# Optimization experiments

Measured on AMD Instinct MI355X. Metric: run time of the kernel, lower is better.

Reference implementation:

```python
import jax, jax.numpy as jnp
import numpy as np

D_MODEL = 512
D_INNER = 1024   # 2 * d_model (Mamba default expand=2)
D_STATE = 16
D_CONV = 4
DT_RANK = 32     # ceil(d_model / 16)
N_LAYERS = 2
EPS = 1e-5


def rmsnorm(x, w):
    return x * jax.lax.rsqrt(jnp.mean(x * x, axis=-1, keepdims=True) + EPS) * w


def silu(x):
    return x * jax.nn.sigmoid(x)


def causal_conv1d(x, w, b):
    # x: [B,S,di], w: [di,d_conv] depthwise, b: [di]; causal left padding
    xt = jnp.transpose(x, (0, 2, 1))                 # [B,di,S]
    k = w[:, None, :]                                # [di,1,k]
    y = jax.lax.conv_general_dilated(
        xt, k, (1,), [(D_CONV - 1, 0)],
        dimension_numbers=('NCH', 'OIH', 'NCH'),
        feature_group_count=D_INNER)
    return jnp.transpose(y, (0, 2, 1)) + b


def selective_scan(u, dt, A, Bm, C, Dp):
    # u,dt: [B,S,di]; Bm,C: [B,S,ds]; A: [di,ds]; Dp: [di]
    def step(h, inp):
        dt_t, B_t, C_t, u_t = inp                    # [B,di],[B,ds],[B,ds],[B,di]
        dA = jnp.exp(dt_t[:, :, None] * A)           # [B,di,ds]
        h = dA * h + (dt_t * u_t)[:, :, None] * B_t[:, None, :]
        y = jnp.einsum('bds,bs->bd', h, C_t)
        return h, y

    B, S, di = u.shape
    h0 = jnp.zeros((B, di, D_STATE), u.dtype)
    xs = (jnp.swapaxes(dt, 0, 1), jnp.swapaxes(Bm, 0, 1),
          jnp.swapaxes(C, 0, 1), jnp.swapaxes(u, 0, 1))
    _, ys = jax.lax.scan(step, h0, xs)               # ys: [S,B,di]
    return jnp.swapaxes(ys, 0, 1) + u * Dp


def mamba_block(x, in_proj, conv_w, conv_b, xproj, dtproj, dtproj_b, A_log, Dp, outproj):
    xz = x @ in_proj.T                               # [B,S,2*di]
    u, z = jnp.split(xz, 2, axis=-1)
    u = silu(causal_conv1d(u, conv_w, conv_b))
    x_dbl = u @ xproj.T                              # [B,S,dt_rank+2*ds]
    dt = jax.nn.softplus(x_dbl[..., :DT_RANK] @ dtproj.T + dtproj_b)
    Bm = x_dbl[..., DT_RANK:DT_RANK + D_STATE]
    C = x_dbl[..., DT_RANK + D_STATE:]
    A = -jnp.exp(A_log)
    y = selective_scan(u, dt, A, Bm, C, Dp)
    return (y * silu(z)) @ outproj.T


def setup_inputs() -> dict:
    key = jax.random.key(0)
    ks = jax.random.split(key, 8)
    B, S, L = 2, 2048, N_LAYERS

    def w(k, shape, s=0.02):
        return jax.random.normal(k, shape, jnp.float32) * s

    inp = {}
    inp['input_data'] = jax.random.normal(ks[0], (B, D_MODEL, S), jnp.float32)
    inp['mask'] = jnp.ones((B, S), jnp.bool_)
    inp['in_proj_w'] = w(ks[1], (L, 2 * D_INNER, D_MODEL))
    inp['conv_w'] = w(ks[2], (L, D_INNER, D_CONV), 0.2)
    inp['conv_b'] = jnp.zeros((L, D_INNER), jnp.float32)
    inp['xproj_w'] = w(ks[3], (L, DT_RANK + 2 * D_STATE, D_INNER))
    inp['dtproj_w'] = w(ks[4], (L, D_INNER, DT_RANK), 0.1)
    inp['dtproj_b'] = w(ks[5], (L, D_INNER), 0.5) - 4.0  # softplus -> small dt
    inp['A_log'] = jnp.log(jnp.broadcast_to(
        jnp.arange(1, D_STATE + 1, dtype=jnp.float32), (L, D_INNER, D_STATE)))
    inp['Dp'] = jnp.ones((L, D_INNER), jnp.float32)
    inp['outproj_w'] = w(ks[6], (L, D_MODEL, D_INNER))
    inp['norm_w'] = jnp.ones((L, D_MODEL), jnp.float32)
    inp['final_norm_w'] = jnp.ones((D_MODEL,), jnp.float32)
    return inp


def reference(input_data, mask, in_proj_w, conv_w, conv_b, xproj_w, dtproj_w,
              dtproj_b, A_log, Dp, outproj_w, norm_w, final_norm_w):
    x = jnp.transpose(input_data, (0, 2, 1))         # [B,S,D]
    for l in range(N_LAYERS):
        x = x + mamba_block(rmsnorm(x, norm_w[l]), in_proj_w[l], conv_w[l],
                            conv_b[l], xproj_w[l], dtproj_w[l], dtproj_b[l],
                            A_log[l], Dp[l], outproj_w[l])
    tokens = rmsnorm(x, final_norm_w)                # [B,S,D] (lm_head=Identity)
    lengths = jnp.sum(mask.astype(jnp.int32), axis=1)
    idx = jnp.maximum(lengths - 1, 0)
    emb = jnp.take_along_axis(tokens, idx[:, None, None], axis=1)[:, 0]  # [B,D]
    return tokens, emb
```

## Files before the change

### kernel.cpp

```cpp
#include <hip/hip_runtime.h>
#include <hip/hip_bf16.h>
#include <cmath>

#define BQ 2
#define SQ 2048
#define DM 512
#define DI 1024
#define DSTATE 16
#define DCONV 4
#define DTR 32
#define NLAYERS 2
#define CHUNK 64
#define NCH (SQ / CHUNK)

typedef __attribute__((ext_vector_type(8))) short bf16x8;
typedef __attribute__((ext_vector_type(4))) float f32x4;

__device__ __forceinline__ unsigned short f2bf(float f) {
    __hip_bfloat16 h = __float2bfloat16(f);
    return *reinterpret_cast<unsigned short*>(&h);
}

__global__ __launch_bounds__(256) void k_transpose(const float* __restrict__ in,
                                                   float* __restrict__ out) {
    __shared__ float tile[32][33];
    int b = blockIdx.z;
    int s0 = blockIdx.x * 32, c0 = blockIdx.y * 32;
    int tx = threadIdx.x, ty = threadIdx.y;
#pragma unroll
    for (int i = 0; i < 4; i++)
        tile[ty + i * 8][tx] = in[((size_t)b * DM + c0 + ty + i * 8) * SQ + s0 + tx];
    __syncthreads();
#pragma unroll
    for (int i = 0; i < 4; i++)
        out[((size_t)b * SQ + s0 + ty + i * 8) * DM + c0 + tx] = tile[tx][ty + i * 8];
}

__global__ __launch_bounds__(256) void k_cvt(const float* __restrict__ in,
                                             unsigned short* __restrict__ out, int n4) {
    int i = blockIdx.x * 256 + threadIdx.x;
    if (i >= n4) return;
    float4 v = ((const float4*)in)[i];
    ushort4 o;
    o.x = f2bf(v.x); o.y = f2bf(v.y); o.z = f2bf(v.z); o.w = f2bf(v.w);
    ((ushort4*)out)[i] = o;
}

__global__ __launch_bounds__(256) void k_rmsnorm_bf(const float* __restrict__ x,
                                                    const float* __restrict__ w,
                                                    unsigned short* __restrict__ out) {
    int row = blockIdx.x;
    const float* xr = x + (size_t)row * DM;
    float v0 = xr[threadIdx.x];
    float v1 = xr[threadIdx.x + 256];
    float ss = v0 * v0 + v1 * v1;
#pragma unroll
    for (int off = 32; off >= 1; off >>= 1) ss += __shfl_xor(ss, off);
    __shared__ float wc[4];
    if ((threadIdx.x & 63) == 0) wc[threadIdx.x >> 6] = ss;
    __syncthreads();
    ss = wc[0] + wc[1] + wc[2] + wc[3];
    float r = rsqrtf(ss * (1.0f / DM) + 1e-5f);
    out[(size_t)row * DM + threadIdx.x] = f2bf(v0 * r * w[threadIdx.x]);
    out[(size_t)row * DM + threadIdx.x + 256] = f2bf(v1 * r * w[threadIdx.x + 256]);
}

__global__ __launch_bounds__(256) void k_rmsnorm_f32(const float* __restrict__ x,
                                                     const float* __restrict__ w,
                                                     float* __restrict__ out) {
    int row = blockIdx.x;
    const float* xr = x + (size_t)row * DM;
    float v0 = xr[threadIdx.x];
    float v1 = xr[threadIdx.x + 256];
    float ss = v0 * v0 + v1 * v1;
#pragma unroll
    for (int off = 32; off >= 1; off >>= 1) ss += __shfl_xor(ss, off);
    __shared__ float wc[4];
    if ((threadIdx.x & 63) == 0) wc[threadIdx.x >> 6] = ss;
    __syncthreads();
    ss = wc[0] + wc[1] + wc[2] + wc[3];
    float r = rsqrtf(ss * (1.0f / DM) + 1e-5f);
    out[(size_t)row * DM + threadIdx.x] = v0 * r * w[threadIdx.x];
    out[(size_t)row * DM + threadIdx.x + 256] = v1 * r * w[threadIdx.x + 256];
}

__global__ __launch_bounds__(256) void k_gemm_bf16(const unsigned short* __restrict__ A, int lda,
                                                   const unsigned short* __restrict__ W, int ldw,
                                                   float* __restrict__ C, int ldc, int K,
                                                   const float* __restrict__ resid, int ldr) {
    __shared__ __align__(16) unsigned short As[128 * 32];
    __shared__ __align__(16) unsigned short Bs[128 * 32];
    const int bm = blockIdx.y * 128, bn = blockIdx.x * 128;
    const int tid = threadIdx.x;
    const int w = tid >> 6, l = tid & 63;
    const int wr = w >> 1, wc = w & 1;
    const int lg = l >> 4, lr16 = l & 15;
    f32x4 acc[4][4] = {};
    for (int k0 = 0; k0 < K; k0 += 32) {
        __syncthreads();
#pragma unroll
        for (int i = 0; i < 2; i++) {
            int slot = i * 256 + tid;
            int row = slot >> 2, s = slot & 3;
            int sg = s ^ (row & 3);
            __builtin_amdgcn_global_load_lds(
                (const __attribute__((address_space(1))) unsigned int*)(A + (size_t)(bm + row) * lda + k0 + sg * 8),
                (__attribute__((address_space(3))) unsigned int*)(As + slot * 8), 16, 0, 0);
            __builtin_amdgcn_global_load_lds(
                (const __attribute__((address_space(1))) unsigned int*)(W + (size_t)(bn + row) * ldw + k0 + sg * 8),
                (__attribute__((address_space(3))) unsigned int*)(Bs + slot * 8), 16, 0, 0);
        }
        asm volatile("s_waitcnt vmcnt(0)" ::: "memory");
        __syncthreads();
        bf16x8 fa[4], fb[4];
#pragma unroll
        for (int f = 0; f < 4; f++) {
            int ar = wr * 64 + f * 16 + lr16;
            fa[f] = *(const bf16x8*)&As[ar * 32 + (lg ^ (ar & 3)) * 8];
            int br = wc * 64 + f * 16 + lr16;
            fb[f] = *(const bf16x8*)&Bs[br * 32 + (lg ^ (br & 3)) * 8];
        }
#pragma unroll
        for (int fi = 0; fi < 4; fi++)
#pragma unroll
            for (int fj = 0; fj < 4; fj++)
                acc[fi][fj] = __builtin_amdgcn_mfma_f32_16x16x32_bf16(fa[fi], fb[fj], acc[fi][fj], 0, 0, 0);
    }
#pragma unroll
    for (int fi = 0; fi < 4; fi++)
#pragma unroll
        for (int fj = 0; fj < 4; fj++)
#pragma unroll
            for (int r = 0; r < 4; r++) {
                int m = bm + wr * 64 + fi * 16 + lg * 4 + r;
                int n = bn + wc * 64 + fj * 16 + lr16;
                float v = acc[fi][fj][r];
                if (resid) v += resid[(size_t)m * ldr + n];
                C[(size_t)m * ldc + n] = v;
            }
}

__global__ __launch_bounds__(256) void k_gemm_bf16_n64(const unsigned short* __restrict__ A, int lda,
                                                       const unsigned short* __restrict__ W, int ldw,
                                                       float* __restrict__ C, int ldc, int K) {
    __shared__ __align__(16) unsigned short As[128 * 32];
    __shared__ __align__(16) unsigned short Bs[64 * 32];
    const int bm = blockIdx.x * 128;
    const int tid = threadIdx.x;
    const int w = tid >> 6, l = tid & 63;
    const int lg = l >> 4, lr16 = l & 15;
    f32x4 acc[2][4] = {};
    for (int k0 = 0; k0 < K; k0 += 32) {
        __syncthreads();
#pragma unroll
        for (int i = 0; i < 2; i++) {
            int slot = i * 256 + tid;
            int row = slot >> 2, s = slot & 3;
            int sg = s ^ (row & 3);
            __builtin_amdgcn_global_load_lds(
                (const __attribute__((address_space(1))) unsigned int*)(A + (size_t)(bm + row) * lda + k0 + sg * 8),
                (__attribute__((address_space(3))) unsigned int*)(As + slot * 8), 16, 0, 0);
        }
        {
            int slot = tid;
            int row = slot >> 2, s = slot & 3;
            int sg = s ^ (row & 3);
            __builtin_amdgcn_global_load_lds(
                (const __attribute__((address_space(1))) unsigned int*)(W + (size_t)row * ldw + k0 + sg * 8),
                (__attribute__((address_space(3))) unsigned int*)(Bs + slot * 8), 16, 0, 0);
        }
        asm volatile("s_waitcnt vmcnt(0)" ::: "memory");
        __syncthreads();
        bf16x8 fa[2], fb[4];
#pragma unroll
        for (int f = 0; f < 2; f++) {
            int ar = w * 32 + f * 16 + lr16;
            fa[f] = *(const bf16x8*)&As[ar * 32 + (lg ^ (ar & 3)) * 8];
        }
#pragma unroll
        for (int f = 0; f < 4; f++) {
            int br = f * 16 + lr16;
            fb[f] = *(const bf16x8*)&Bs[br * 32 + (lg ^ (br & 3)) * 8];
        }
#pragma unroll
        for (int fi = 0; fi < 2; fi++)
#pragma unroll
            for (int fj = 0; fj < 4; fj++)
                acc[fi][fj] = __builtin_amdgcn_mfma_f32_16x16x32_bf16(fa[fi], fb[fj], acc[fi][fj], 0, 0, 0);
    }
#pragma unroll
    for (int fi = 0; fi < 2; fi++)
#pragma unroll
        for (int fj = 0; fj < 4; fj++)
#pragma unroll
            for (int r = 0; r < 4; r++) {
                int m = bm + w * 32 + fi * 16 + lg * 4 + r;
                int n = fj * 16 + lr16;
                C[(size_t)m * ldc + n] = acc[fi][fj][r];
            }
}

__global__ __launch_bounds__(256) void k_gemm(const float* __restrict__ A, int lda,
                                              const float* __restrict__ W, int ldw,
                                              float* __restrict__ C, int ldc, int K,
                                              const float* __restrict__ bias, int act,
                                              const float* __restrict__ resid, int ldr) {
    __shared__ float As[16][64];
    __shared__ float Bs[16][64];
    int bm = blockIdx.y * 64, bn = blockIdx.x * 64;
    int tid = threadIdx.x;
    int tx = tid & 15, ty = tid >> 4;
    int lr = tid >> 2, lk = (tid & 3) << 2;
    float acc[4][4] = {};
    for (int k0 = 0; k0 < K; k0 += 16) {
        float4 av = *(const float4*)&A[(size_t)(bm + lr) * lda + k0 + lk];
        float4 wv = *(const float4*)&W[(size_t)(bn + lr) * ldw + k0 + lk];
        __syncthreads();
        As[lk + 0][lr] = av.x; As[lk + 1][lr] = av.y;
        As[lk + 2][lr] = av.z; As[lk + 3][lr] = av.w;
        Bs[lk + 0][lr] = wv.x; Bs[lk + 1][lr] = wv.y;
        Bs[lk + 2][lr] = wv.z; Bs[lk + 3][lr] = wv.w;
        __syncthreads();
#pragma unroll
        for (int k = 0; k < 16; k++) {
            float a[4], bb[4];
#pragma unroll
            for (int i = 0; i < 4; i++) a[i] = As[k][ty * 4 + i];
#pragma unroll
            for (int j = 0; j < 4; j++) bb[j] = Bs[k][tx * 4 + j];
#pragma unroll
            for (int i = 0; i < 4; i++)
#pragma unroll
                for (int j = 0; j < 4; j++) acc[i][j] += a[i] * bb[j];
        }
    }
#pragma unroll
    for (int i = 0; i < 4; i++) {
        int m = bm + ty * 4 + i;
#pragma unroll
        for (int j = 0; j < 4; j++) {
            int n = bn + tx * 4 + j;
            float v = acc[i][j];
            if (bias) v += bias[n];
            if (act == 1) v = fmaxf(v, 0.f) + log1pf(expf(-fabsf(v)));
            if (resid) v += resid[(size_t)m * ldr + n];
            C[(size_t)m * ldc + n] = v;
        }
    }
}

__global__ __launch_bounds__(256) void k_conv_silu(const float* __restrict__ xz,
                                                   const float* __restrict__ cw,
                                                   const float* __restrict__ cb,
                                                   float* __restrict__ u,
                                                   unsigned short* __restrict__ ubf) {
    int bt = blockIdx.x;
    int t = bt & (SQ - 1);
#pragma unroll
    for (int dd = 0; dd < 4; dd++) {
        int d = dd * 256 + threadIdx.x;
        float acc = cb[d];
#pragma unroll
        for (int k = 0; k < DCONV; k++) {
            int tk = t + k - (DCONV - 1);
            if (tk >= 0)
                acc += xz[((size_t)(bt + k - (DCONV - 1))) * (2 * DI) + d] * cw[d * DCONV + k];
        }
        float sig = 1.f / (1.f + expf(-acc));
        float v = acc * sig;
        u[(size_t)bt * DI + d] = v;
        ubf[(size_t)bt * DI + d] = f2bf(v);
    }
}

__global__ __launch_bounds__(256) void k_scan_p1(const float* __restrict__ xdbl,
                                                 const float* __restrict__ dt,
                                                 const float* __restrict__ u,
                                                 const float* __restrict__ A_log,
                                                 float* __restrict__ hend,
                                                 float* __restrict__ dchunk) {
    int bc = blockIdx.x >> 4;
    int d0 = (blockIdx.x & 15) << 6;
    int b = bc >> 5;
    int c = bc & (NCH - 1);
    int tid = threadIdx.x;
    int q = tid & 3, dl = tid >> 2;
    int d = d0 + dl;
    float4 av = *(const float4*)&A_log[((size_t)d << 4) + 4 * q];
    float a0 = -expf(av.x), a1 = -expf(av.y), a2 = -expf(av.z), a3 = -expf(av.w);
    float h0 = 0.f, h1 = 0.f, h2 = 0.f, h3 = 0.f, sumdt = 0.f;
    __shared__ float sdt[32][65], su[32][65];
    __shared__ __align__(16) float sB[32][16];
    int tbase = c * CHUNK;
    for (int t0 = 0; t0 < CHUNK; t0 += 32) {
        __syncthreads();
#pragma unroll
        for (int i = 0; i < 8; i++) {
            int e = i * 256 + tid;
            int tt = e >> 6, j = e & 63;
            size_t rowm = (size_t)(b * SQ + tbase + t0 + tt);
            sdt[tt][j] = dt[rowm * DI + d0 + j];
            su[tt][j]  = u[rowm * DI + d0 + j];
        }
#pragma unroll
        for (int i = 0; i < 2; i++) {
            int e = i * 256 + tid;
            int tt = e >> 4, j = e & 15;
            size_t rowm = (size_t)(b * SQ + tbase + t0 + tt);
            sB[tt][j] = xdbl[rowm * 64 + DTR + j];
        }
        __syncthreads();
        for (int tt = 0; tt < 32; tt++) {
            float dtv = sdt[tt][dl], uv = su[tt][dl];
            float dtu = dtv * uv;
            sumdt += dtv;
            float4 Bv = *(const float4*)&sB[tt][4 * q];
            h0 = __expf(dtv * a0) * h0 + dtu * Bv.x;
            h1 = __expf(dtv * a1) * h1 + dtu * Bv.y;
            h2 = __expf(dtv * a2) * h2 + dtu * Bv.z;
            h3 = __expf(dtv * a3) * h3 + dtu * Bv.w;
        }
    }
    size_t o = ((size_t)bc << 14) + ((size_t)d << 4) + 4 * q;
    *(float4*)&hend[o] = make_float4(h0, h1, h2, h3);
    *(float4*)&dchunk[o] = make_float4(__expf(a0 * sumdt), __expf(a1 * sumdt),
                                       __expf(a2 * sumdt), __expf(a3 * sumdt));
}

__global__ __launch_bounds__(256) void k_scan_p2(const float* __restrict__ hend,
                                                 const float* __restrict__ dchunk,
                                                 float* __restrict__ hstart) {
    int tid = blockIdx.x * 256 + threadIdx.x;
    int b = tid >> 14;
    int ds = tid & 16383;
    float h = 0.f;
#pragma unroll
    for (int c = 0; c < NCH; c++) {
        size_t o = (((size_t)(b * NCH + c)) << 14) + ds;
        hstart[o] = h;
        h = dchunk[o] * h + hend[o];
    }
}

__global__ __launch_bounds__(256) void k_scan_p3(const float* __restrict__ xdbl,
                                                 const float* __restrict__ dt,
                                                 const float* __restrict__ u,
                                                 const float* __restrict__ xz,
                                                 const float* __restrict__ A_log,
                                                 const float* __restrict__ Dp,
                                                 const float* __restrict__ hstart,
                                                 unsigned short* __restrict__ yout) {
    int bc = blockIdx.x >> 4;
    int d0 = (blockIdx.x & 15) << 6;
    int b = bc >> 5;
    int c = bc & (NCH - 1);
    int tid = threadIdx.x;
    int q = tid & 3, dl = tid >> 2;
    int d = d0 + dl;
    float4 av = *(const float4*)&A_log[((size_t)d << 4) + 4 * q];
    float a0 = -expf(av.x), a1 = -expf(av.y), a2 = -expf(av.z), a3 = -expf(av.w);
    size_t o = ((size_t)bc << 14) + ((size_t)d << 4) + 4 * q;
    float4 hv = *(const float4*)&hstart[o];
    float h0 = hv.x, h1 = hv.y, h2 = hv.z, h3 = hv.w;
    float Dv = Dp[d];
    __shared__ float sdt[32][65], su[32][65], sz[32][65];
    __shared__ __align__(16) float sBC[32][32];
    int tbase = c * CHUNK;
    for (int t0 = 0; t0 < CHUNK; t0 += 32) {
        __syncthreads();
#pragma unroll
        for (int i = 0; i < 8; i++) {
            int e = i * 256 + tid;
            int tt = e >> 6, j = e & 63;
            size_t rowm = (size_t)(b * SQ + tbase + t0 + tt);
            sdt[tt][j] = dt[rowm * DI + d0 + j];
            su[tt][j]  = u[rowm * DI + d0 + j];
            sz[tt][j]  = xz[rowm * (2 * DI) + DI + d0 + j];
        }
#pragma unroll
        for (int i = 0; i < 4; i++) {
            int e = i * 256 + tid;
            int tt = e >> 5, j = e & 31;
            size_t rowm = (size_t)(b * SQ + tbase + t0 + tt);
            sBC[tt][j] = xdbl[rowm * 64 + DTR + j];
        }
        __syncthreads();
        for (int tt = 0; tt < 32; tt++) {
            float dtv = sdt[tt][dl], uv = su[tt][dl];
            float dtu = dtv * uv;
            float4 Bv = *(const float4*)&sBC[tt][4 * q];
            float4 Cv = *(const float4*)&sBC[tt][16 + 4 * q];
            h0 = __expf(dtv * a0) * h0 + dtu * Bv.x;
            h1 = __expf(dtv * a1) * h1 + dtu * Bv.y;
            h2 = __expf(dtv * a2) * h2 + dtu * Bv.z;
            h3 = __expf(dtv * a3) * h3 + dtu * Bv.w;
            float y = h0 * Cv.x + h1 * Cv.y + h2 * Cv.z + h3 * Cv.w;
            y += __shfl_xor(y, 1);
            y += __shfl_xor(y, 2);
            if (q == 0) {
                y += uv * Dv;
                float zv = sz[tt][dl];
                float g = zv / (1.f + __expf(-zv));
                yout[(size_t)(b * SQ + tbase + t0 + tt) * DI + d] = f2bf(y * g);
            }
        }
    }
}

__global__ __launch_bounds__(256) void k_emb(const float* __restrict__ tokens,
                                             const int* __restrict__ mask,
                                             float* __restrict__ emb) {
    int b = blockIdx.x;
    int cnt = 0;
    for (int i = threadIdx.x; i < SQ; i += 256) cnt += mask[b * SQ + i] ? 1 : 0;
#pragma unroll
    for (int off = 32; off >= 1; off >>= 1) cnt += __shfl_xor(cnt, off);
    __shared__ int wc[4];
    if ((threadIdx.x & 63) == 0) wc[threadIdx.x >> 6] = cnt;
    __syncthreads();
    int total = wc[0] + wc[1] + wc[2] + wc[3];
    int idx = total > 0 ? total - 1 : 0;
    for (int i = threadIdx.x; i < DM; i += 256)
        emb[b * DM + i] = tokens[((size_t)b * SQ + idx) * DM + i];
}

extern "C" void kernel_launch(void* const* d_in, const int* in_sizes, int n_in,
                              void* d_out, int out_size, void* d_ws, size_t ws_size,
                              hipStream_t stream) {
    const float* input_data   = (const float*)d_in[0];
    const int*   mask         = (const int*)d_in[1];
    const float* in_proj_w    = (const float*)d_in[2];
    const float* conv_w       = (const float*)d_in[3];
    const float* conv_b       = (const float*)d_in[4];
    const float* xproj_w      = (const float*)d_in[5];
    const float* dtproj_w     = (const float*)d_in[6];
    const float* dtproj_b     = (const float*)d_in[7];
    const float* A_log        = (const float*)d_in[8];
    const float* Dp           = (const float*)d_in[9];
    const float* outproj_w    = (const float*)d_in[10];
    const float* norm_w       = (const float*)d_in[11];
    const float* final_norm_w = (const float*)d_in[12];
    float* out = (float*)d_out;

    const size_t M = (size_t)BQ * SQ;
    const size_t CS = (size_t)BQ * NCH * DI * DSTATE;
    float* x              = (float*)d_ws;
    unsigned short* xn_bf = (unsigned short*)(x + M * DM);
    float* xz             = (float*)(xn_bf + M * DM);
    float* u              = xz + M * 2 * DI;
    float* xdbl           = u + M * DI;
    float* dtb            = xdbl + M * 64;
    unsigned short* ubf   = (unsigned short*)(dtb + M * DI);
    unsigned short* ybf   = ubf + M * DI;
    float* hend           = (float*)(ybf + M * DI);
    float* dchunk         = hend + CS;
    float* hstart         = dchunk + CS;
    unsigned short* wbf_in  = (unsigned short*)(hstart + CS);
    unsigned short* wbf_out = wbf_in + (size_t)NLAYERS * 2 * DI * DM;
    unsigned short* wbf_x   = wbf_out + (size_t)NLAYERS * DM * DI;

    {
        int n4 = NLAYERS * 2 * DI * DM / 4;
        k_cvt<<<(n4 + 255) / 256, 256, 0, stream>>>(in_proj_w, wbf_in, n4);
        n4 = NLAYERS * DM * DI / 4;
        k_cvt<<<(n4 + 255) / 256, 256, 0, stream>>>(outproj_w, wbf_out, n4);
        n4 = NLAYERS * 64 * DI / 4;
        k_cvt<<<(n4 + 255) / 256, 256, 0, stream>>>(xproj_w, wbf_x, n4);
    }

    k_transpose<<<dim3(SQ / 32, DM / 32, BQ), dim3(32, 8), 0, stream>>>(input_data, x);

    for (int l = 0; l < NLAYERS; l++) {
        k_rmsnorm_bf<<<M, 256, 0, stream>>>(x, norm_w + (size_t)l * DM, xn_bf);
        k_gemm_bf16<<<dim3(2 * DI / 128, M / 128), 256, 0, stream>>>(
            xn_bf, DM, wbf_in + (size_t)l * 2 * DI * DM, DM, xz, 2 * DI, DM,
            nullptr, 0);
        k_conv_silu<<<M, 256, 0, stream>>>(xz, conv_w + (size_t)l * DI * DCONV,
                                           conv_b + (size_t)l * DI, u, ubf);
        k_gemm_bf16_n64<<<M / 128, 256, 0, stream>>>(
            ubf, DI, wbf_x + (size_t)l * 64 * DI, DI, xdbl, 64, DI);
        k_gemm<<<dim3(DI / 64, M / 64), 256, 0, stream>>>(
            xdbl, 64, dtproj_w + (size_t)l * DI * DTR, DTR, dtb, DI, DTR,
            dtproj_b + (size_t)l * DI, 1, nullptr, 0);
        k_scan_p1<<<BQ * NCH * (DI / 64), 256, 0, stream>>>(
            xdbl, dtb, u, A_log + (size_t)l * DI * DSTATE, hend, dchunk);
        k_scan_p2<<<(BQ * DI * DSTATE) / 256, 256, 0, stream>>>(hend, dchunk, hstart);
        k_scan_p3<<<BQ * NCH * (DI / 64), 256, 0, stream>>>(
            xdbl, dtb, u, xz, A_log + (size_t)l * DI * DSTATE, Dp + (size_t)l * DI,
            hstart, ybf);
        k_gemm_bf16<<<dim3(DM / 128, M / 128), 256, 0, stream>>>(
            ybf, DI, wbf_out + (size_t)l * DM * DI, DI, x, DM, DI,
            x, DM);
    }

    k_rmsnorm_f32<<<M, 256, 0, stream>>>(x, final_norm_w, out);
    k_emb<<<BQ, 256, 0, stream>>>(out, mask, out + M * DM);
}
```

Measured before the change: 468.6 us.

## Template bf16 MFMA GEMM, split-K x_proj, sliding-window conv, vectorized scan loads

```diff
diff --git a/kernel.cpp b/kernel.cpp
--- a/kernel.cpp
+++ b/kernel.cpp
@@ -12,6 +12,7 @@
 #define NLAYERS 2
 #define CHUNK 64
 #define NCH (SQ / CHUNK)
+#define LOG2E 1.4426950408889634f
 
 typedef __attribute__((ext_vector_type(8))) short bf16x8;
 typedef __attribute__((ext_vector_type(4))) float f32x4;
@@ -84,19 +85,87 @@
     out[(size_t)row * DM + threadIdx.x + 256] = v1 * r * w[threadIdx.x + 256];
 }
 
-__global__ __launch_bounds__(256) void k_gemm_bf16(const unsigned short* __restrict__ A, int lda,
-                                                   const unsigned short* __restrict__ W, int ldw,
-                                                   float* __restrict__ C, int ldc, int K,
-                                                   const float* __restrict__ resid, int ldr) {
-    __shared__ __align__(16) unsigned short As[128 * 32];
-    __shared__ __align__(16) unsigned short Bs[128 * 32];
-    const int bm = blockIdx.y * 128, bn = blockIdx.x * 128;
+template<int BM, int BN, int AFR, int BFR>
+__global__ __launch_bounds__(256) void k_gemm_bf16_t(const unsigned short* __restrict__ A, int lda,
+                                                     const unsigned short* __restrict__ W, int ldw,
+                                                     float* __restrict__ C, int ldc, int K,
+                                                     const float* __restrict__ bias, int act,
+                                                     const float* __restrict__ resid, int ldr) {
+    __shared__ __align__(16) unsigned short As[BM * 32];
+    __shared__ __align__(16) unsigned short Bs[BN * 32];
+    const int bm = blockIdx.y * BM, bn = blockIdx.x * BN;
     const int tid = threadIdx.x;
     const int w = tid >> 6, l = tid & 63;
     const int wr = w >> 1, wc = w & 1;
     const int lg = l >> 4, lr16 = l & 15;
-    f32x4 acc[4][4] = {};
+    f32x4 acc[AFR][BFR] = {};
     for (int k0 = 0; k0 < K; k0 += 32) {
+        __syncthreads();
+#pragma unroll
+        for (int i = 0; i < BM / 64; i++) {
+            int slot = i * 256 + tid;
+            int row = slot >> 2, s = slot & 3;
+            int sg = s ^ (row & 3);
+            __builtin_amdgcn_global_load_lds(
+                (const __attribute__((address_space(1))) unsigned int*)(A + (size_t)(bm + row) * lda + k0 + sg * 8),
+                (__attribute__((address_space(3))) unsigned int*)(As + slot * 8), 16, 0, 0);
+        }
+#pragma unroll
+        for (int i = 0; i < BN / 64; i++) {
+            int slot = i * 256 + tid;
+            int row = slot >> 2, s = slot & 3;
+            int sg = s ^ (row & 3);
+            __builtin_amdgcn_global_load_lds(
+                (const __attribute__((address_space(1))) unsigned int*)(W + (size_t)(bn + row) * ldw + k0 + sg * 8),
+                (__attribute__((address_space(3))) unsigned int*)(Bs + slot * 8), 16, 0, 0);
+        }
+        asm volatile("s_waitcnt vmcnt(0)" ::: "memory");
+        __syncthreads();
+        bf16x8 fa[AFR], fb[BFR];
+#pragma unroll
+        for (int f = 0; f < AFR; f++) {
+            int ar = wr * (BM / 2) + f * 16 + lr16;
+            fa[f] = *(const bf16x8*)&As[ar * 32 + (lg ^ (ar & 3)) * 8];
+        }
+#pragma unroll
+        for (int f = 0; f < BFR; f++) {
+            int br = wc * (BN / 2) + f * 16 + lr16;
+            fb[f] = *(const bf16x8*)&Bs[br * 32 + (lg ^ (br & 3)) * 8];
+        }
+#pragma unroll
+        for (int fi = 0; fi < AFR; fi++)
+#pragma unroll
+            for (int fj = 0; fj < BFR; fj++)
+                acc[fi][fj] = __builtin_amdgcn_mfma_f32_16x16x32_bf16(fa[fi], fb[fj], acc[fi][fj], 0, 0, 0);
+    }
+#pragma unroll
+    for (int fi = 0; fi < AFR; fi++)
+#pragma unroll
+        for (int fj = 0; fj < BFR; fj++)
+#pragma unroll
+            for (int r = 0; r < 4; r++) {
+                int m = bm + wr * (BM / 2) + fi * 16 + lg * 4 + r;
+                int n = bn + wc * (BN / 2) + fj * 16 + lr16;
+                float v = acc[fi][fj][r];
+                if (bias) v += bias[n];
+                if (act == 1) v = fmaxf(v, 0.f) + log1pf(expf(-fabsf(v)));
+                if (resid) v += resid[(size_t)m * ldr + n];
+                C[(size_t)m * ldc + n] = v;
+            }
+}
+
+__global__ __launch_bounds__(256) void k_gemm_n64_sk(const unsigned short* __restrict__ A, int lda,
+                                                     const unsigned short* __restrict__ W, int ldw,
+                                                     float* __restrict__ part) {
+    __shared__ __align__(16) unsigned short As[128 * 32];
+    __shared__ __align__(16) unsigned short Bs[64 * 32];
+    const int bm = blockIdx.x * 128;
+    const int koff = blockIdx.y * 128;
+    const int tid = threadIdx.x;
+    const int w = tid >> 6, l = tid & 63;
+    const int lg = l >> 4, lr16 = l & 15;
+    f32x4 acc[2][4] = {};
+    for (int k0 = koff; k0 < koff + 128; k0 += 32) {
         __syncthreads();
 #pragma unroll
         for (int i = 0; i < 2; i++) {
@@ -106,60 +175,6 @@
             __builtin_amdgcn_global_load_lds(
                 (const __attribute__((address_space(1))) unsigned int*)(A + (size_t)(bm + row) * lda + k0 + sg * 8),
                 (__attribute__((address_space(3))) unsigned int*)(As + slot * 8), 16, 0, 0);
-            __builtin_amdgcn_global_load_lds(
-                (const __attribute__((address_space(1))) unsigned int*)(W + (size_t)(bn + row) * ldw + k0 + sg * 8),
-                (__attribute__((address_space(3))) unsigned int*)(Bs + slot * 8), 16, 0, 0);
-        }
-        asm volatile("s_waitcnt vmcnt(0)" ::: "memory");
-        __syncthreads();
-        bf16x8 fa[4], fb[4];
-#pragma unroll
-        for (int f = 0; f < 4; f++) {
-            int ar = wr * 64 + f * 16 + lr16;
-            fa[f] = *(const bf16x8*)&As[ar * 32 + (lg ^ (ar & 3)) * 8];
-            int br = wc * 64 + f * 16 + lr16;
-            fb[f] = *(const bf16x8*)&Bs[br * 32 + (lg ^ (br & 3)) * 8];
-        }
-#pragma unroll
-        for (int fi = 0; fi < 4; fi++)
-#pragma unroll
-            for (int fj = 0; fj < 4; fj++)
-                acc[fi][fj] = __builtin_amdgcn_mfma_f32_16x16x32_bf16(fa[fi], fb[fj], acc[fi][fj], 0, 0, 0);
-    }
-#pragma unroll
-    for (int fi = 0; fi < 4; fi++)
-#pragma unroll
-        for (int fj = 0; fj < 4; fj++)
-#pragma unroll
-            for (int r = 0; r < 4; r++) {
-                int m = bm + wr * 64 + fi * 16 + lg * 4 + r;
-                int n = bn + wc * 64 + fj * 16 + lr16;
-                float v = acc[fi][fj][r];
-                if (resid) v += resid[(size_t)m * ldr + n];
-                C[(size_t)m * ldc + n] = v;
-            }
-}
-
-__global__ __launch_bounds__(256) void k_gemm_bf16_n64(const unsigned short* __restrict__ A, int lda,
-                                                       const unsigned short* __restrict__ W, int ldw,
-                                                       float* __restrict__ C, int ldc, int K) {
-    __shared__ __align__(16) unsigned short As[128 * 32];
-    __shared__ __align__(16) unsigned short Bs[64 * 32];
-    const int bm = blockIdx.x * 128;
-    const int tid = threadIdx.x;
-    const int w = tid >> 6, l = tid & 63;
-    const int lg = l >> 4, lr16 = l & 15;
-    f32x4 acc[2][4] = {};
-    for (int k0 = 0; k0 < K; k0 += 32) {
-        __syncthreads();
-#pragma unroll
-        for (int i = 0; i < 2; i++) {
-            int slot = i * 256 + tid;
-            int row = slot >> 2, s = slot & 3;
-            int sg = s ^ (row & 3);
-            __builtin_amdgcn_global_load_lds(
-                (const __attribute__((address_space(1))) unsigned int*)(A + (size_t)(bm + row) * lda + k0 + sg * 8),
-                (__attribute__((address_space(3))) unsigned int*)(As + slot * 8), 16, 0, 0);
         }
         {
             int slot = tid;
@@ -188,6 +203,7 @@
             for (int fj = 0; fj < 4; fj++)
                 acc[fi][fj] = __builtin_amdgcn_mfma_f32_16x16x32_bf16(fa[fi], fb[fj], acc[fi][fj], 0, 0, 0);
     }
+    float* out = part + (size_t)blockIdx.y * ((size_t)BQ * SQ * 64);
 #pragma unroll
     for (int fi = 0; fi < 2; fi++)
 #pragma unroll
@@ -196,57 +212,26 @@
             for (int r = 0; r < 4; r++) {
                 int m = bm + w * 32 + fi * 16 + lg * 4 + r;
                 int n = fj * 16 + lr16;
-                C[(size_t)m * ldc + n] = acc[fi][fj][r];
+                out[(size_t)m * 64 + n] = acc[fi][fj][r];
             }
 }
 
-__global__ __launch_bounds__(256) void k_gemm(const float* __restrict__ A, int lda,
-                                              const float* __restrict__ W, int ldw,
-                                              float* __restrict__ C, int ldc, int K,
-                                              const float* __restrict__ bias, int act,
-                                              const float* __restrict__ resid, int ldr) {
-    __shared__ float As[16][64];
-    __shared__ float Bs[16][64];
-    int bm = blockIdx.y * 64, bn = blockIdx.x * 64;
-    int tid = threadIdx.x;
-    int tx = tid & 15, ty = tid >> 4;
-    int lr = tid >> 2, lk = (tid & 3) << 2;
-    float acc[4][4] = {};
-    for (int k0 = 0; k0 < K; k0 += 16) {
-        float4 av = *(const float4*)&A[(size_t)(bm + lr) * lda + k0 + lk];
-        float4 wv = *(const float4*)&W[(size_t)(bn + lr) * ldw + k0 + lk];
-        __syncthreads();
-        As[lk + 0][lr] = av.x; As[lk + 1][lr] = av.y;
-        As[lk + 2][lr] = av.z; As[lk + 3][lr] = av.w;
-        Bs[lk + 0][lr] = wv.x; Bs[lk + 1][lr] = wv.y;
-        Bs[lk + 2][lr] = wv.z; Bs[lk + 3][lr] = wv.w;
-        __syncthreads();
-#pragma unroll
-        for (int k = 0; k < 16; k++) {
-            float a[4], bb[4];
-#pragma unroll
-            for (int i = 0; i < 4; i++) a[i] = As[k][ty * 4 + i];
-#pragma unroll
-            for (int j = 0; j < 4; j++) bb[j] = Bs[k][tx * 4 + j];
-#pragma unroll
-            for (int i = 0; i < 4; i++)
-#pragma unroll
-                for (int j = 0; j < 4; j++) acc[i][j] += a[i] * bb[j];
-        }
-    }
-#pragma unroll
-    for (int i = 0; i < 4; i++) {
-        int m = bm + ty * 4 + i;
-#pragma unroll
-        for (int j = 0; j < 4; j++) {
-            int n = bn + tx * 4 + j;
-            float v = acc[i][j];
-            if (bias) v += bias[n];
-            if (act == 1) v = fmaxf(v, 0.f) + log1pf(expf(-fabsf(v)));
-            if (resid) v += resid[(size_t)m * ldr + n];
-            C[(size_t)m * ldc + n] = v;
-        }
-    }
+__global__ __launch_bounds__(256) void k_xdbl_reduce(const float* __restrict__ part,
+                                                     float* __restrict__ xdbl,
+                                                     unsigned short* __restrict__ xbf) {
+    const int n4 = BQ * SQ * 64 / 4;
+    int i = blockIdx.x * 256 + threadIdx.x;
+    if (i >= n4) return;
+    float4 s = ((const float4*)part)[i];
+#pragma unroll
+    for (int ks = 1; ks < 8; ks++) {
+        float4 t = ((const float4*)part)[(size_t)ks * n4 + i];
+        s.x += t.x; s.y += t.y; s.z += t.z; s.w += t.w;
+    }
+    ((float4*)xdbl)[i] = s;
+    ushort4 o;
+    o.x = f2bf(s.x); o.y = f2bf(s.y); o.z = f2bf(s.z); o.w = f2bf(s.w);
+    ((ushort4*)xbf)[i] = o;
 }
 
 __global__ __launch_bounds__(256) void k_conv_silu(const float* __restrict__ xz,
@@ -254,22 +239,28 @@
                                                    const float* __restrict__ cb,
                                                    float* __restrict__ u,
                                                    unsigned short* __restrict__ ubf) {
-    int bt = blockIdx.x;
-    int t = bt & (SQ - 1);
-#pragma unroll
-    for (int dd = 0; dd < 4; dd++) {
-        int d = dd * 256 + threadIdx.x;
-        float acc = cb[d];
-#pragma unroll
-        for (int k = 0; k < DCONV; k++) {
-            int tk = t + k - (DCONV - 1);
-            if (tk >= 0)
-                acc += xz[((size_t)(bt + k - (DCONV - 1))) * (2 * DI) + d] * cw[d * DCONV + k];
-        }
-        float sig = 1.f / (1.f + expf(-acc));
-        float v = acc * sig;
-        u[(size_t)bt * DI + d] = v;
-        ubf[(size_t)bt * DI + d] = f2bf(v);
+    int b = blockIdx.z;
+    int t0 = blockIdx.x * 64;
+    int d = blockIdx.y * 256 + threadIdx.x;
+    float4 wv = ((const float4*)cw)[d];
+    float bias = cb[d];
+    const size_t rs = 2 * DI;
+    size_t base = (size_t)b * SQ * rs + d;
+    float x0 = 0.f, x1 = 0.f, x2 = 0.f;
+    if (t0 > 0) {
+        x0 = xz[base + (size_t)(t0 - 3) * rs];
+        x1 = xz[base + (size_t)(t0 - 2) * rs];
+        x2 = xz[base + (size_t)(t0 - 1) * rs];
+    }
+    for (int t = t0; t < t0 + 64; t++) {
+        float x3 = xz[base + (size_t)t * rs];
+        float a = bias + wv.x * x0 + wv.y * x1 + wv.z * x2 + wv.w * x3;
+        float sig = 1.f / (1.f + __expf(-a));
+        float v = a * sig;
+        size_t o = (size_t)(b * SQ + t) * DI + d;
+        u[o] = v;
+        ubf[o] = f2bf(v);
+        x0 = x1; x1 = x2; x2 = x3;
     }
 }
 
@@ -287,27 +278,26 @@
     int q = tid & 3, dl = tid >> 2;
     int d = d0 + dl;
     float4 av = *(const float4*)&A_log[((size_t)d << 4) + 4 * q];
-    float a0 = -expf(av.x), a1 = -expf(av.y), a2 = -expf(av.z), a3 = -expf(av.w);
+    float a0 = -expf(av.x) * LOG2E, a1 = -expf(av.y) * LOG2E;
+    float a2 = -expf(av.z) * LOG2E, a3 = -expf(av.w) * LOG2E;
     float h0 = 0.f, h1 = 0.f, h2 = 0.f, h3 = 0.f, sumdt = 0.f;
-    __shared__ float sdt[32][65], su[32][65];
-    __shared__ __align__(16) float sB[32][16];
+    __shared__ __align__(16) float sdt[32][68], su[32][68];
+    __shared__ __align__(16) float sB[32][20];
     int tbase = c * CHUNK;
     for (int t0 = 0; t0 < CHUNK; t0 += 32) {
         __syncthreads();
 #pragma unroll
-        for (int i = 0; i < 8; i++) {
-            int e = i * 256 + tid;
-            int tt = e >> 6, j = e & 63;
-            size_t rowm = (size_t)(b * SQ + tbase + t0 + tt);
-            sdt[tt][j] = dt[rowm * DI + d0 + j];
-            su[tt][j]  = u[rowm * DI + d0 + j];
-        }
-#pragma unroll
         for (int i = 0; i < 2; i++) {
             int e = i * 256 + tid;
-            int tt = e >> 4, j = e & 15;
+            int tt = e >> 4, j4 = e & 15;
             size_t rowm = (size_t)(b * SQ + tbase + t0 + tt);
-            sB[tt][j] = xdbl[rowm * 64 + DTR + j];
+            *(float4*)&sdt[tt][j4 * 4] = *(const float4*)&dt[rowm * DI + d0 + j4 * 4];
+            *(float4*)&su[tt][j4 * 4]  = *(const float4*)&u[rowm * DI + d0 + j4 * 4];
+        }
+        if (tid < 128) {
+            int tt = tid >> 2, j4 = tid & 3;
+            size_t rowm = (size_t)(b * SQ + tbase + t0 + tt);
+            *(float4*)&sB[tt][j4 * 4] = *(const float4*)&xdbl[rowm * 64 + DTR + j4 * 4];
         }
         __syncthreads();
         for (int tt = 0; tt < 32; tt++) {
@@ -315,16 +305,16 @@
             float dtu = dtv * uv;
             sumdt += dtv;
             float4 Bv = *(const float4*)&sB[tt][4 * q];
-            h0 = __expf(dtv * a0) * h0 + dtu * Bv.x;
-            h1 = __expf(dtv * a1) * h1 + dtu * Bv.y;
-            h2 = __expf(dtv * a2) * h2 + dtu * Bv.z;
-            h3 = __expf(dtv * a3) * h3 + dtu * Bv.w;
+            h0 = exp2f(dtv * a0) * h0 + dtu * Bv.x;
+            h1 = exp2f(dtv * a1) * h1 + dtu * Bv.y;
+            h2 = exp2f(dtv * a2) * h2 + dtu * Bv.z;
+            h3 = exp2f(dtv * a3) * h3 + dtu * Bv.w;
         }
     }
     size_t o = ((size_t)bc << 14) + ((size_t)d << 4) + 4 * q;
     *(float4*)&hend[o] = make_float4(h0, h1, h2, h3);
-    *(float4*)&dchunk[o] = make_float4(__expf(a0 * sumdt), __expf(a1 * sumdt),
-                                       __expf(a2 * sumdt), __expf(a3 * sumdt));
+    *(float4*)&dchunk[o] = make_float4(exp2f(a0 * sumdt), exp2f(a1 * sumdt),
+                                       exp2f(a2 * sumdt), exp2f(a3 * sumdt));
 }
 
 __global__ __launch_bounds__(256) void k_scan_p2(const float* __restrict__ hend,
@@ -358,31 +348,30 @@
     int q = tid & 3, dl = tid >> 2;
     int d = d0 + dl;
     float4 av = *(const float4*)&A_log[((size_t)d << 4) + 4 * q];
-    float a0 = -expf(av.x), a1 = -expf(av.y), a2 = -expf(av.z), a3 = -expf(av.w);
+    float a0 = -expf(av.x) * LOG2E, a1 = -expf(av.y) * LOG2E;
+    float a2 = -expf(av.z) * LOG2E, a3 = -expf(av.w) * LOG2E;
     size_t o = ((size_t)bc << 14) + ((size_t)d << 4) + 4 * q;
     float4 hv = *(const float4*)&hstart[o];
     float h0 = hv.x, h1 = hv.y, h2 = hv.z, h3 = hv.w;
     float Dv = Dp[d];
-    __shared__ float sdt[32][65], su[32][65], sz[32][65];
-    __shared__ __align__(16) float sBC[32][32];
+    __shared__ __align__(16) float sdt[32][68], su[32][68], sz[32][68];
+    __shared__ __align__(16) float sBC[32][36];
     int tbase = c * CHUNK;
     for (int t0 = 0; t0 < CHUNK; t0 += 32) {
         __syncthreads();
 #pragma unroll
-        for (int i = 0; i < 8; i++) {
+        for (int i = 0; i < 2; i++) {
             int e = i * 256 + tid;
-            int tt = e >> 6, j = e & 63;
+            int tt = e >> 4, j4 = e & 15;
             size_t rowm = (size_t)(b * SQ + tbase + t0 + tt);
-            sdt[tt][j] = dt[rowm * DI + d0 + j];
-            su[tt][j]  = u[rowm * DI + d0 + j];
-            sz[tt][j]  = xz[rowm * (2 * DI) + DI + d0 + j];
-        }
-#pragma unroll
-        for (int i = 0; i < 4; i++) {
-            int e = i * 256 + tid;
-            int tt = e >> 5, j = e & 31;
+            *(float4*)&sdt[tt][j4 * 4] = *(const float4*)&dt[rowm * DI + d0 + j4 * 4];
+            *(float4*)&su[tt][j4 * 4]  = *(const float4*)&u[rowm * DI + d0 + j4 * 4];
+            *(float4*)&sz[tt][j4 * 4]  = *(const float4*)&xz[rowm * (2 * DI) + DI + d0 + j4 * 4];
+        }
+        {
+            int tt = tid >> 3, j4 = tid & 7;
             size_t rowm = (size_t)(b * SQ + tbase + t0 + tt);
-            sBC[tt][j] = xdbl[rowm * 64 + DTR + j];
+            *(float4*)&sBC[tt][j4 * 4] = *(const float4*)&xdbl[rowm * 64 + DTR + j4 * 4];
         }
         __syncthreads();
         for (int tt = 0; tt < 32; tt++) {
@@ -390,10 +379,10 @@
             float dtu = dtv * uv;
             float4 Bv = *(const float4*)&sBC[tt][4 * q];
             float4 Cv = *(const float4*)&sBC[tt][16 + 4 * q];
-            h0 = __expf(dtv * a0) * h0 + dtu * Bv.x;
-            h1 = __expf(dtv * a1) * h1 + dtu * Bv.y;
-            h2 = __expf(dtv * a2) * h2 + dtu * Bv.z;
-            h3 = __expf(dtv * a3) * h3 + dtu * Bv.w;
+            h0 = exp2f(dtv * a0) * h0 + dtu * Bv.x;
+            h1 = exp2f(dtv * a1) * h1 + dtu * Bv.y;
+            h2 = exp2f(dtv * a2) * h2 + dtu * Bv.z;
+            h3 = exp2f(dtv * a3) * h3 + dtu * Bv.w;
             float y = h0 * Cv.x + h1 * Cv.y + h2 * Cv.z + h3 * Cv.w;
             y += __shfl_xor(y, 1);
             y += __shfl_xor(y, 2);
@@ -455,9 +444,12 @@
     float* hend           = (float*)(ybf + M * DI);
     float* dchunk         = hend + CS;
     float* hstart         = dchunk + CS;
-    unsigned short* wbf_in  = (unsigned short*)(hstart + CS);
+    float* xpart          = hstart + CS;
+    unsigned short* xdbl_bf = (unsigned short*)(xpart + 8 * M * 64);
+    unsigned short* wbf_in  = xdbl_bf + M * 64;
     unsigned short* wbf_out = wbf_in + (size_t)NLAYERS * 2 * DI * DM;
     unsigned short* wbf_x   = wbf_out + (size_t)NLAYERS * DM * DI;
+    unsigned short* wbf_dt  = wbf_x + (size_t)NLAYERS * 64 * DI;
 
     {
         int n4 = NLAYERS * 2 * DI * DM / 4;
@@ -466,21 +458,25 @@
         k_cvt<<<(n4 + 255) / 256, 256, 0, stream>>>(outproj_w, wbf_out, n4);
         n4 = NLAYERS * 64 * DI / 4;
         k_cvt<<<(n4 + 255) / 256, 256, 0, stream>>>(xproj_w, wbf_x, n4);
+        n4 = NLAYERS * DI * DTR / 4;
+        k_cvt<<<(n4 + 255) / 256, 256, 0, stream>>>(dtproj_w, wbf_dt, n4);
     }
 
     k_transpose<<<dim3(SQ / 32, DM / 32, BQ), dim3(32, 8), 0, stream>>>(input_data, x);
 
     for (int l = 0; l < NLAYERS; l++) {
         k_rmsnorm_bf<<<M, 256, 0, stream>>>(x, norm_w + (size_t)l * DM, xn_bf);
-        k_gemm_bf16<<<dim3(2 * DI / 128, M / 128), 256, 0, stream>>>(
+        k_gemm_bf16_t<128, 128, 4, 4><<<dim3(2 * DI / 128, M / 128), 256, 0, stream>>>(
             xn_bf, DM, wbf_in + (size_t)l * 2 * DI * DM, DM, xz, 2 * DI, DM,
-            nullptr, 0);
-        k_conv_silu<<<M, 256, 0, stream>>>(xz, conv_w + (size_t)l * DI * DCONV,
-                                           conv_b + (size_t)l * DI, u, ubf);
-        k_gemm_bf16_n64<<<M / 128, 256, 0, stream>>>(
-            ubf, DI, wbf_x + (size_t)l * 64 * DI, DI, xdbl, 64, DI);
-        k_gemm<<<dim3(DI / 64, M / 64), 256, 0, stream>>>(
-            xdbl, 64, dtproj_w + (size_t)l * DI * DTR, DTR, dtb, DI, DTR,
+            nullptr, 0, nullptr, 0);
+        k_conv_silu<<<dim3(SQ / 64, DI / 256, BQ), 256, 0, stream>>>(
+            xz, conv_w + (size_t)l * DI * DCONV, conv_b + (size_t)l * DI, u, ubf);
+        k_gemm_n64_sk<<<dim3(M / 128, 8), 256, 0, stream>>>(
+            ubf, DI, wbf_x + (size_t)l * 64 * DI, DI, xpart);
+        k_xdbl_reduce<<<(BQ * SQ * 64 / 4 + 255) / 256, 256, 0, stream>>>(
+            xpart, xdbl, xdbl_bf);
+        k_gemm_bf16_t<64, 128, 2, 4><<<dim3(DI / 128, M / 64), 256, 0, stream>>>(
+            xdbl_bf, 64, wbf_dt + (size_t)l * DI * DTR, DTR, dtb, DI, DTR,
             dtproj_b + (size_t)l * DI, 1, nullptr, 0);
         k_scan_p1<<<BQ * NCH * (DI / 64), 256, 0, stream>>>(
             xdbl, dtb, u, A_log + (size_t)l * DI * DSTATE, hend, dchunk);
@@ -488,9 +484,9 @@
         k_scan_p3<<<BQ * NCH * (DI / 64), 256, 0, stream>>>(
             xdbl, dtb, u, xz, A_log + (size_t)l * DI * DSTATE, Dp + (size_t)l * DI,
             hstart, ybf);
-        k_gemm_bf16<<<dim3(DM / 128, M / 128), 256, 0, stream>>>(
+        k_gemm_bf16_t<64, 128, 2, 4><<<dim3(DM / 128, M / 64), 256, 0, stream>>>(
             ybf, DI, wbf_out + (size_t)l * DM * DI, DI, x, DM, DI,
-            x, DM);
+            nullptr, 0, x, DM);
     }
 
     k_rmsnorm_f32<<<M, 256, 0, stream>>>(x, final_norm_w, out);
```

Result: no change. 473.7 us (+1.1%).
